# Kernel optimization log

Hardware: AMD Instinct MI355X
Metric: run time of the kernel (lower is better)

## Reference

```python
import jax, jax.numpy as jnp
import numpy as np

N = 1024          # number of rois (single image)
C = 1024          # in_channels
G = 16            # num_groups
PE = 64           # position_embedding_channels
WAVE_LENGTH = 1000.0


def _position_embedding(bboxes, pe_channels, wave_length):
    # bboxes: [N, 4] xyxy. Pairwise geometric features vs all (nongt == all) boxes.
    x1, y1, x2, y2 = jnp.split(bboxes, 4, axis=1)          # each [N,1]
    cx = (x1 + x2) * 0.5
    cy = (y1 + y2) * 0.5
    w = x2 - x1 + 1.0
    h = y2 - y1 + 1.0
    dX = jnp.log(jnp.clip(jnp.abs((cx - cx.T) / w), 1e-3))  # [N,N]
    dY = jnp.log(jnp.clip(jnp.abs((cy - cy.T) / h), 1e-3))
    dW = jnp.log(w / w.T)
    dH = jnp.log(h / h.T)
    pm = jnp.stack([dX, dY, dW, dH], axis=-1)               # [N,N,4]
    feat_range = jnp.arange(pe_channels // 8, dtype=pm.dtype)
    dim_mat = jnp.power(jnp.asarray(wave_length, pm.dtype),
                        (8.0 / pe_channels) * feat_range)    # [pe//8]
    div = (100.0 * pm)[..., None] / dim_mat                  # [N,N,4,pe//8]
    emb = jnp.concatenate([jnp.sin(div), jnp.cos(div)], axis=3)  # [N,N,4,pe//4]
    return emb.reshape(emb.shape[0], emb.shape[1], -1)       # [N,N,pe]


def setup_inputs() -> dict:
    key = jax.random.key(0)
    ks = jax.random.split(key, 10)
    feats = jax.random.normal(ks[0], (N, C), dtype=jnp.float32)
    # realistic boxes: x1,y1 in [0,800), w,h in [1,200)
    x1 = jax.random.uniform(ks[1], (N, 1), minval=0.0, maxval=800.0)
    y1 = jax.random.uniform(ks[2], (N, 1), minval=0.0, maxval=800.0)
    bw = jax.random.uniform(ks[3], (N, 1), minval=1.0, maxval=200.0)
    bh = jax.random.uniform(ks[4], (N, 1), minval=1.0, maxval=200.0)
    rois = jnp.concatenate([jnp.zeros((N, 1)), x1, y1, x1 + bw, y1 + bh], axis=1).astype(jnp.float32)
    Wq = 0.01 * jax.random.normal(ks[5], (C, C), dtype=jnp.float32)
    bq = jnp.zeros((C,), jnp.float32)
    Wk = 0.01 * jax.random.normal(ks[6], (C, C), dtype=jnp.float32)
    bk = jnp.zeros((C,), jnp.float32)
    Wg = 0.01 * jax.random.normal(ks[7], (G, PE), dtype=jnp.float32)   # 1x1 conv PE->G
    bg = jnp.zeros((G,), jnp.float32)
    # grouped 1x1 conv: in=G*C, out=C, groups=G -> weight [C, C]
    limit = np.sqrt(6.0 / (C + C))
    Wv = jax.random.uniform(ks[8], (C, C), minval=-limit, maxval=limit, dtype=jnp.float32)
    bv = jnp.zeros((C,), jnp.float32)
    return {"feats": feats, "rois": rois, "Wq": Wq, "bq": bq, "Wk": Wk, "bk": bk,
            "Wg": Wg, "bg": bg, "Wv": Wv, "bv": bv}


def reference(feats, rois, Wq, bq, Wk, bk, Wg, bg, Wv, bv):
    n, c = feats.shape
    g = Wg.shape[0]
    gc = c // g
    # position embedding computed under no_grad in torch
    emb = jax.lax.stop_gradient(_position_embedding(rois[:, 1:5], Wg.shape[1], WAVE_LENGTH))  # [N,N,PE]
    # 1x1 conv w_g + relu -> geometric attention weight [N, G, M]
    aff_weight = jax.nn.relu(jnp.einsum('nmp,gp->ngm', emb, Wg) + bg[None, :, None])
    q = (feats @ Wq.T + bq).reshape(n, g, gc)   # [N,G,gc]
    k = (feats @ Wk.T + bk).reshape(n, g, gc)   # [M,G,gc] (nongt == all)
    scale = 1.0 / jnp.sqrt(jnp.asarray(gc, jnp.float32))
    aff = jnp.einsum('ngc,mgc->ngm', q, k) * scale            # [N,G,M]
    weighted = jnp.log(jnp.clip(aff_weight, 1e-6)) + aff
    sm = jax.nn.softmax(weighted, axis=2)                      # [N,G,M]
    out = jnp.einsum('ngm,mc->ngc', sm, feats)                 # [N,G,C]
    # grouped 1x1 conv w_v: group g maps its C-dim aggregate to gc channels
    Wv_g = Wv.reshape(g, gc, c)
    rel = jnp.einsum('ngc,gdc->ngd', out, Wv_g).reshape(n, c) + bv
    return rel
```

## Files before the change

### kernel.cpp

```cpp
#include <hip/hip_runtime.h>
#include <math.h>

#define N_ROIS 1024
#define C_DIM  1024

typedef __attribute__((ext_vector_type(8))) short short8;
typedef __attribute__((ext_vector_type(4))) float f32x4;

__device__ __forceinline__ unsigned short f2bf(float x) {
    union { float f; unsigned u; } v; v.f = x;
    unsigned r = v.u + 0x7fffu + ((v.u >> 16) & 1u);
    return (unsigned short)(r >> 16);
}
__device__ __forceinline__ float bf2f(unsigned short u) {
    return __uint_as_float((unsigned)u << 16);
}
__device__ __forceinline__ unsigned cvtpk(float lo, float hi) {
    unsigned r;
    asm("v_cvt_pk_bf16_f32 %0, %1, %2" : "=v"(r) : "v"(lo), "v"(hi));
    return r;
}

__global__ __launch_bounds__(256) void cvt_kernel(
    const float* __restrict__ s0, const float* __restrict__ s1,
    const float* __restrict__ s2, const float* __restrict__ s3,
    unsigned short* __restrict__ d0, unsigned short* __restrict__ d1,
    unsigned short* __restrict__ d2, unsigned short* __restrict__ d3)
{
    const float* s; unsigned short* d;
    switch (blockIdx.y) {
        case 0:  s = s0; d = d0; break;
        case 1:  s = s1; d = d1; break;
        case 2:  s = s2; d = d2; break;
        default: s = s3; d = d3; break;
    }
    const int i = (blockIdx.x * 256 + threadIdx.x) * 8;
    float4 a = *(const float4*)&s[i];
    float4 b = *(const float4*)&s[i + 4];
    uint4 o;
    o.x = cvtpk(a.x, a.y); o.y = cvtpk(a.z, a.w);
    o.z = cvtpk(b.x, b.y); o.w = cvtpk(b.z, b.w);
    *(uint4*)&d[i] = o;
}

struct Triples {
    const unsigned short* A[3];
    const unsigned short* B[3];
    unsigned short*       C[3];
    const float*          bias[3];
};

__global__ __launch_bounds__(256) void prep_kernel(
    Triples tr, const float* __restrict__ rois, const float* __restrict__ Wg,
    const float* __restrict__ bg, unsigned short* __restrict__ logw)
{
    __shared__ __align__(16) char smem[52224];
    const int bx = blockIdx.x;
    const int t  = threadIdx.x;

    if (bx < 192) {
        constexpr int LDT = 40;
        unsigned short* As = (unsigned short*)smem;
        unsigned short* Bs = As + 128 * LDT;
        const int z   = bx >> 6;
        const int rem = bx & 63;
        const int m0 = (rem >> 3) * 128, n0 = (rem & 7) * 128;
        const unsigned short* A = tr.A[z];
        const unsigned short* B = tr.B[z];
        f32x4 acc[4][4];
        const f32x4 z4 = {0.f, 0.f, 0.f, 0.f};
#pragma unroll
        for (int i = 0; i < 4; ++i)
#pragma unroll
            for (int j = 0; j < 4; ++j) acc[i][j] = z4;

        const int row = t >> 2;
        const int kc  = (t & 3) * 8;
        const unsigned short* gA0 = A + (size_t)(m0 + row) * 1024 + kc;
        const unsigned short* gA1 = gA0 + (size_t)64 * 1024;
        unsigned short* sA0 = &As[row * LDT + kc];
        unsigned short* sA1 = sA0 + 64 * LDT;
        const unsigned short* gB0 = B + (size_t)(n0 + row) * 1024 + kc;
        const unsigned short* gB1 = gB0 + (size_t)64 * 1024;
        unsigned short* sB0 = &Bs[row * LDT + kc];
        unsigned short* sB1 = sB0 + 64 * LDT;
        int4 ra0 = *(const int4*)gA0;
        int4 ra1 = *(const int4*)gA1;
        int4 rb0 = *(const int4*)gB0;
        int4 rb1 = *(const int4*)gB1;
        const int lane = t & 63, wid = t >> 6;
        const int wm = (wid & 1) * 64, wn = (wid >> 1) * 64;
        const unsigned short* pa = &As[(wm + (lane & 15)) * LDT + (lane >> 4) * 8];
        const unsigned short* pb = &Bs[(wn + (lane & 15)) * LDT + (lane >> 4) * 8];
        for (int k0 = 0; k0 < 1024; k0 += 32) {
            *(int4*)sA0 = ra0; *(int4*)sA1 = ra1;
            *(int4*)sB0 = rb0; *(int4*)sB1 = rb1;
            __syncthreads();
            if (k0 + 32 < 1024) {
                ra0 = *(const int4*)(gA0 + k0 + 32);
                ra1 = *(const int4*)(gA1 + k0 + 32);
                rb0 = *(const int4*)(gB0 + k0 + 32);
                rb1 = *(const int4*)(gB1 + k0 + 32);
            }
            short8 af[4], bfr[4];
#pragma unroll
            for (int mi = 0; mi < 4; ++mi) af[mi]  = *(const short8*)(pa + mi * 16 * LDT);
#pragma unroll
            for (int ni = 0; ni < 4; ++ni) bfr[ni] = *(const short8*)(pb + ni * 16 * LDT);
#pragma unroll
            for (int mi = 0; mi < 4; ++mi)
#pragma unroll
                for (int ni = 0; ni < 4; ++ni)
                    acc[mi][ni] = __builtin_amdgcn_mfma_f32_16x16x32_bf16(
                        af[mi], bfr[ni], acc[mi][ni], 0, 0, 0);
            __syncthreads();
        }
        const float* bias = tr.bias[z];
        unsigned short* C = tr.C[z];
        const float sc = (z == 0) ? 0.125f : 1.0f;
        const int r0 = (lane >> 4) * 4, cc = lane & 15;
#pragma unroll
        for (int mi = 0; mi < 4; ++mi)
#pragma unroll
            for (int ni = 0; ni < 4; ++ni) {
                const int col = n0 + wn + ni * 16 + cc;
                const float bb = bias ? bias[col] : 0.f;
                const int rowi = m0 + wm + mi * 16 + r0;
                const unsigned p01 = cvtpk((acc[mi][ni][0] + bb) * sc,
                                           (acc[mi][ni][1] + bb) * sc);
                const unsigned p23 = cvtpk((acc[mi][ni][2] + bb) * sc,
                                           (acc[mi][ni][3] + bb) * sc);
                C[(size_t)rowi * 1024 + col]       = (unsigned short)(p01 & 0xffff);
                C[(size_t)(rowi + 1) * 1024 + col] = (unsigned short)(p01 >> 16);
                C[(size_t)(rowi + 2) * 1024 + col] = (unsigned short)(p23 & 0xffff);
                C[(size_t)(rowi + 3) * 1024 + col] = (unsigned short)(p23 >> 16);
            }
    } else {
        unsigned short* wg_s = (unsigned short*)smem;
        float* bg_s = (float*)(smem + 2304);
        float (*mbox)[4] = (float(*)[4])(smem + 2368);
        const int w = t >> 6, lane = t & 63;
        unsigned short* ptile = (unsigned short*)(smem + 18752) + w * 4160;
        if (t < 128) {
            const int gi = t >> 3, c = (t & 7) * 8;
            unsigned short* d = &wg_s[gi * 72 + c];
#pragma unroll
            for (int u = 0; u < 8; ++u) d[u] = f2bf(Wg[gi * 64 + c + u]);
        }
        if (t < 16) bg_s[t] = bg[t];
#pragma unroll
        for (int i = 0; i < 4; ++i) {
            const int m = t + i * 256;
            const float x1 = rois[m * 5 + 1], y1 = rois[m * 5 + 2];
            const float x2 = rois[m * 5 + 3], y2 = rois[m * 5 + 4];
            mbox[m][0] = (x1 + x2) * 0.5f;
            mbox[m][1] = (y1 + y2) * 0.5f;
            mbox[m][2] = __logf(x2 - x1 + 1.f);
            mbox[m][3] = __logf(y2 - y1 + 1.f);
        }
        const int n = bx - 192;
        const float x1 = rois[n * 5 + 1], y1 = rois[n * 5 + 2];
        const float x2 = rois[n * 5 + 3], y2 = rois[n * 5 + 4];
        const float cxn = (x1 + x2) * 0.5f, cyn = (y1 + y2) * 0.5f;
        const float wn = x2 - x1 + 1.f, hn = y2 - y1 + 1.f;
        const float iwn = 1.f / wn, ihn = 1.f / hn;
        const float lwn = __logf(wn), lhn = __logf(hn);
        __syncthreads();

        const int g  = lane & 15;
        const int qw = lane >> 4;
        const float coff = (qw & 1) ? 1.5707963268f : 0.f;
        const int f0 = qw >> 1;
        const short8 bf0 = *(const short8*)&wg_s[g * 72 + qw * 8];
        const short8 bf1 = *(const short8*)&wg_s[g * 72 + qw * 8 + 32];
        const float bgv = bg_s[g];
        const float invd[8] = {1.f, 0.42169650342f, 0.1778279410f, 0.07498942093f,
                               0.0316227766f, 0.01333521432f, 0.005623413252f, 0.002371373706f};

        for (int cl = 0; cl < 16; ++cl) {
            const int c  = w * 16 + cl;
            const int ma = c * 16 + g;
            float4 mb = *(const float4*)&mbox[ma][0];
            float p0 = (f0 == 0)
                     ? __logf(fmaxf(fabsf((cxn - mb.x) * iwn), 1e-3f))
                     : __logf(fmaxf(fabsf((cyn - mb.y) * ihn), 1e-3f));
            float p1 = (f0 == 0) ? (lwn - mb.z) : (lhn - mb.w);
            p0 *= 100.f; p1 *= 100.f;
            float s0v[8], s1v[8];
#pragma unroll
            for (int rr = 0; rr < 8; ++rr) {
                s0v[rr] = __sinf(p0 * invd[rr] + coff);
                s1v[rr] = __sinf(p1 * invd[rr] + coff);
            }
            union { uint4 u; short8 s; } a0, a1;
            a0.u.x = cvtpk(s0v[0], s0v[1]); a0.u.y = cvtpk(s0v[2], s0v[3]);
            a0.u.z = cvtpk(s0v[4], s0v[5]); a0.u.w = cvtpk(s0v[6], s0v[7]);
            a1.u.x = cvtpk(s1v[0], s1v[1]); a1.u.y = cvtpk(s1v[2], s1v[3]);
            a1.u.z = cvtpk(s1v[4], s1v[5]); a1.u.w = cvtpk(s1v[6], s1v[7]);
            f32x4 acc = {0.f, 0.f, 0.f, 0.f};
            acc = __builtin_amdgcn_mfma_f32_16x16x32_bf16(a0.s, bf0, acc, 0, 0, 0);
            acc = __builtin_amdgcn_mfma_f32_16x16x32_bf16(a1.s, bf1, acc, 0, 0, 0);
            const float l0 = __logf(fmaxf(acc[0] + bgv, 1e-6f));
            const float l1 = __logf(fmaxf(acc[1] + bgv, 1e-6f));
            const float l2 = __logf(fmaxf(acc[2] + bgv, 1e-6f));
            const float l3 = __logf(fmaxf(acc[3] + bgv, 1e-6f));
            uint2 pk;
            pk.x = cvtpk(l0, l1);
            pk.y = cvtpk(l2, l3);
            *(uint2*)&ptile[g * 260 + cl * 16 + qw * 4] = pk;
        }
        unsigned short* outp = logw + (size_t)n * 16384 + w * 256;
#pragma unroll
        for (int gg = 0; gg < 16; ++gg) {
            const uint2 pv = *(const uint2*)&ptile[gg * 260 + lane * 4];
            *(uint2*)&outp[gg * 1024 + lane * 4] = pv;
        }
    }
}

#define QOFF 0
#define KOFF 8192
#define FOFF 24576
#define LOFF 40960
#define POFF 57344
#define PPAD 72

__global__ __launch_bounds__(256) void attn_kernel(
    const unsigned short* __restrict__ qb, const unsigned short* __restrict__ kb,
    const unsigned short* __restrict__ logw, const unsigned short* __restrict__ FWt,
    const float* __restrict__ bv, float* __restrict__ out)
{
    __shared__ __align__(16) char smem[66560];

    const int t = threadIdx.x;
    const int bid = blockIdx.x;
    const int g  = (bid & 7) * 2 + ((bid >> 3) >> 4);
    const int n0 = ((bid >> 3) & 15) * 64;

    const int lane = t & 63, W = t >> 6;
    const int qw = lane >> 4, lx = lane & 15;
    const int lx7 = lx & 7;
    const int r8 = lane >> 3, u = lane & 7;

#define GLD(srcp, ldsoff) __builtin_amdgcn_global_load_lds( \
        (const __attribute__((address_space(1))) void*)(srcp), \
        (__attribute__((address_space(3))) void*)(smem + (ldsoff)), 16, 0, 0)

#pragma unroll
    for (int j = 0; j < 2; ++j) {
        const int c = W * 2 + j;
        const int r = c * 8 + r8;
        GLD(qb + (size_t)(n0 + r) * 1024 + g * 64 + ((u ^ (r & 7)) * 8),
            QOFF + c * 1024);
        GLD(kb + (size_t)r * 1024 + g * 64 + ((u ^ (r & 7)) * 8),
            KOFF + c * 1024);
        GLD(FWt + (size_t)(g * 64 + r) * 1024 + ((u ^ (r & 7)) * 8),
            FOFF + c * 1024);
        GLD(logw + (size_t)(n0 + r) * 16384 + g * 1024 + (((2 * u) ^ (r & 6)) * 4),
            LOFF + c * 1024);
    }
    __syncthreads();

    const unsigned short* qS = (const unsigned short*)(smem + QOFF);
    const int qrow = W * 16 + lx;
    const short8 bq0 = *(const short8*)(qS + qrow * 64 + ((qw ^ lx7) * 8));
    const short8 bq1 = *(const short8*)(qS + qrow * 64 + (((qw + 4) ^ lx7) * 8));
    unsigned short* Pw = (unsigned short*)(smem + POFF) + W * 16 * PPAD;

    f32x4 acc[4];
    const f32x4 z4 = {0.f, 0.f, 0.f, 0.f};
#pragma unroll
    for (int nb = 0; nb < 4; ++nb) acc[nb] = z4;
    float mrow = -1e30f, srow = 0.f;

    for (int i = 0; i < 16; ++i) {
        const int cur = i & 1;
        if (i < 15) {
            const int mc = (i + 1) * 64;
            const int nxt = cur ^ 1;
#pragma unroll
            for (int j = 0; j < 2; ++j) {
                const int c = W * 2 + j;
                const int r = c * 8 + r8;
                GLD(kb + (size_t)(mc + r) * 1024 + g * 64 + ((u ^ (r & 7)) * 8),
                    KOFF + nxt * 8192 + c * 1024);
                GLD(FWt + (size_t)(g * 64 + r) * 1024 + mc + ((u ^ (r & 7)) * 8),
                    FOFF + nxt * 8192 + c * 1024);
                GLD(logw + (size_t)(n0 + r) * 16384 + g * 1024 + mc
                        + (((2 * u) ^ (r & 6)) * 4),
                    LOFF + nxt * 8192 + c * 1024);
            }
        }

        const unsigned short* Kc = (const unsigned short*)(smem + KOFF + cur * 8192);
        const unsigned short* Fc = (const unsigned short*)(smem + FOFF + cur * 8192);
        const unsigned short* Lc = (const unsigned short*)(smem + LOFF + cur * 8192);

        f32x4 s[4];
#pragma unroll
        for (int tt = 0; tt < 4; ++tt) {
            const unsigned short* kr = Kc + (tt * 16 + lx) * 64;
            short8 a0 = *(const short8*)(kr + ((qw ^ lx7) * 8));
            short8 a1 = *(const short8*)(kr + (((qw + 4) ^ lx7) * 8));
            f32x4 z = z4;
            z = __builtin_amdgcn_mfma_f32_16x16x32_bf16(a0, bq0, z, 0, 0, 0);
            s[tt] = __builtin_amdgcn_mfma_f32_16x16x32_bf16(a1, bq1, z, 0, 0, 0);
        }

        const unsigned short* Lr = Lc + (W * 16 + lx) * 64;
        float v[4][4];
        float cmx = -1e30f;
#pragma unroll
        for (int tt = 0; tt < 4; ++tt) {
            const int off = ((tt * 32 + qw * 8) ^ ((lx & 6) << 3)) >> 1;
            const uint2 lw = *(const uint2*)(Lr + off);
            v[tt][0] = s[tt][0] + bf2f((unsigned short)(lw.x & 0xffff));
            v[tt][1] = s[tt][1] + bf2f((unsigned short)(lw.x >> 16));
            v[tt][2] = s[tt][2] + bf2f((unsigned short)(lw.y & 0xffff));
            v[tt][3] = s[tt][3] + bf2f((unsigned short)(lw.y >> 16));
            cmx = fmaxf(cmx, fmaxf(fmaxf(v[tt][0], v[tt][1]), fmaxf(v[tt][2], v[tt][3])));
        }
        cmx = fmaxf(cmx, __shfl_xor(cmx, 16));
        cmx = fmaxf(cmx, __shfl_xor(cmx, 32));

        const float nm = fmaxf(mrow, cmx);
        const float f  = __expf(mrow - nm);
        mrow = nm;
        srow *= f;
#pragma unroll
        for (int nb = 0; nb < 4; ++nb) {
            acc[nb][0] *= f; acc[nb][1] *= f;
            acc[nb][2] *= f; acc[nb][3] *= f;
        }

#pragma unroll
        for (int tt = 0; tt < 4; ++tt) {
            const float p0 = __expf(v[tt][0] - nm);
            const float p1 = __expf(v[tt][1] - nm);
            const float p2 = __expf(v[tt][2] - nm);
            const float p3 = __expf(v[tt][3] - nm);
            srow += (p0 + p1) + (p2 + p3);
            uint2 pk;
            pk.x = cvtpk(p0, p1);
            pk.y = cvtpk(p2, p3);
            *(uint2*)&Pw[lx * PPAD + tt * 16 + qw * 4] = pk;
        }

#pragma unroll
        for (int ks = 0; ks < 2; ++ks) {
            const short8 ap = *(const short8*)&Pw[lx * PPAD + ks * 32 + qw * 8];
#pragma unroll
            for (int nb = 0; nb < 4; ++nb) {
                const unsigned short* fr = Fc + (nb * 16 + lx) * 64;
                short8 fb = *(const short8*)(fr + (((ks * 4 + qw) ^ lx7) * 8));
                acc[nb] = __builtin_amdgcn_mfma_f32_16x16x32_bf16(fb, ap, acc[nb], 0, 0, 0);
            }
        }

        __syncthreads();
    }

    srow += __shfl_xor(srow, 16);
    srow += __shfl_xor(srow, 32);
    const float inv = 1.f / srow;
    float* Ow = (float*)smem + W * 16 * 68;
#pragma unroll
    for (int nb = 0; nb < 4; ++nb)
#pragma unroll
        for (int r = 0; r < 4; ++r)
            Ow[lx * 68 + nb * 16 + qw * 4 + r] = acc[nb][r] * inv;
    {
        const int row = lane >> 2, d0 = (lane & 3) * 16;
        const float* Orow = (float*)smem + W * 16 * 68 + row * 68;
        float* op = out + (size_t)(n0 + W * 16 + row) * 1024 + g * 64 + d0;
#pragma unroll
        for (int j = 0; j < 4; ++j) {
            float4 o = *(const float4*)(Orow + d0 + j * 4);
            const float4 b4 = *(const float4*)&bv[g * 64 + d0 + j * 4];
            o.x += b4.x; o.y += b4.y; o.z += b4.z; o.w += b4.w;
            *(float4*)(op + j * 4) = o;
        }
    }
#undef GLD
}

extern "C" void kernel_launch(void* const* d_in, const int* in_sizes, int n_in,
                              void* d_out, int out_size, void* d_ws, size_t ws_size,
                              hipStream_t stream)
{
    const float* feats = (const float*)d_in[0];
    const float* rois  = (const float*)d_in[1];
    const float* Wq    = (const float*)d_in[2];
    const float* bq    = (const float*)d_in[3];
    const float* Wk    = (const float*)d_in[4];
    const float* bk    = (const float*)d_in[5];
    const float* Wg    = (const float*)d_in[6];
    const float* bg    = (const float*)d_in[7];
    const float* Wv    = (const float*)d_in[8];
    const float* bv    = (const float*)d_in[9];
    float* out = (float*)d_out;

    char* wsb = (char*)d_ws;
    unsigned short* logwb  = (unsigned short*)(wsb + (0ull  << 20));
    unsigned short* featsb = (unsigned short*)(wsb + (64ull << 20));
    unsigned short* qb     = (unsigned short*)(wsb + (66ull << 20));
    unsigned short* kb     = (unsigned short*)(wsb + (68ull << 20));
    unsigned short* FWtb   = (unsigned short*)(wsb + (70ull << 20));
    unsigned short* Wqb    = (unsigned short*)(wsb + (80ull << 20));
    unsigned short* Wkb    = (unsigned short*)(wsb + (82ull << 20));
    unsigned short* Wvb    = (unsigned short*)(wsb + (84ull << 20));

    cvt_kernel<<<dim3(512, 4), 256, 0, stream>>>(feats, Wq, Wk, Wv,
                                                 featsb, Wqb, Wkb, Wvb);

    Triples tr;
    tr.A[0] = featsb; tr.B[0] = Wqb;    tr.C[0] = qb;   tr.bias[0] = bq;
    tr.A[1] = featsb; tr.B[1] = Wkb;    tr.C[1] = kb;   tr.bias[1] = bk;
    tr.A[2] = Wvb;    tr.B[2] = featsb; tr.C[2] = FWtb; tr.bias[2] = nullptr;
    prep_kernel<<<1216, 256, 0, stream>>>(tr, rois, Wg, bg, logwb);

    attn_kernel<<<256, 256, 0, stream>>>(qb, kb, logwb, FWtb, bv, out);
}
```

Baseline: 64.93 us.

## Fuse weight bf16 conversion into GEMM loads and split position embedding kernel

Drops the separate conversion kernel. Weights are now converted from fp32 to bf16 inside the GEMM load path, and the feats conversion moves into a new position-embedding kernel. The old combined prep kernel is split in two: a 1024-block pos_kernel, with each block handling four rois against a 256-column slice, and a separate 8x8x3 GEMM kernel that depends on featsb. This removes a pass that wrote bf16 weights out and read them back, but the GEMM now reads fp32 weights (double the bytes), and the GEMMs no longer run concurrently with the embedding work in the same launch.

```diff
diff --git a/kernel.cpp b/kernel.cpp
--- a/kernel.cpp
+++ b/kernel.cpp
@@ -20,202 +20,222 @@
     asm("v_cvt_pk_bf16_f32 %0, %1, %2" : "=v"(r) : "v"(lo), "v"(hi));
     return r;
 }
-
-__global__ __launch_bounds__(256) void cvt_kernel(
-    const float* __restrict__ s0, const float* __restrict__ s1,
-    const float* __restrict__ s2, const float* __restrict__ s3,
-    unsigned short* __restrict__ d0, unsigned short* __restrict__ d1,
-    unsigned short* __restrict__ d2, unsigned short* __restrict__ d3)
+__device__ __forceinline__ int4 ldcvt(const float* p) {
+    float4 f0 = *(const float4*)p;
+    float4 f1 = *(const float4*)(p + 4);
+    int4 r;
+    r.x = (int)cvtpk(f0.x, f0.y); r.y = (int)cvtpk(f0.z, f0.w);
+    r.z = (int)cvtpk(f1.x, f1.y); r.w = (int)cvtpk(f1.z, f1.w);
+    return r;
+}
+
+__global__ __launch_bounds__(256) void pos_kernel(
+    const float* __restrict__ rois, const float* __restrict__ Wg,
+    const float* __restrict__ bg, const float* __restrict__ feats,
+    unsigned short* __restrict__ featsb, unsigned short* __restrict__ logw)
 {
-    const float* s; unsigned short* d;
-    switch (blockIdx.y) {
-        case 0:  s = s0; d = d0; break;
-        case 1:  s = s1; d = d1; break;
-        case 2:  s = s2; d = d2; break;
-        default: s = s3; d = d3; break;
-    }
-    const int i = (blockIdx.x * 256 + threadIdx.x) * 8;
-    float4 a = *(const float4*)&s[i];
-    float4 b = *(const float4*)&s[i + 4];
-    uint4 o;
-    o.x = cvtpk(a.x, a.y); o.y = cvtpk(a.z, a.w);
-    o.z = cvtpk(b.x, b.y); o.w = cvtpk(b.z, b.w);
-    *(uint4*)&d[i] = o;
-}
-
-struct Triples {
-    const unsigned short* A[3];
-    const unsigned short* B[3];
-    unsigned short*       C[3];
-    const float*          bias[3];
+    __shared__ unsigned short wg_s[16 * 72];
+    __shared__ float bg_s[16];
+    __shared__ float mbox[256][4];
+    __shared__ unsigned short ptile[4][2240];
+
+    const int t  = threadIdx.x;
+    const int pb = blockIdx.x;
+    const int ngrp = pb >> 2;
+    const int mc   = (pb & 3) * 256;
+    const int lane = t & 63, w = t >> 6;
+    const int g = lane & 15, qw = lane >> 4;
+
+    {
+        const int i = pb * 1024 + t * 4;
+        float4 a = *(const float4*)&feats[i];
+        uint2 o;
+        o.x = cvtpk(a.x, a.y); o.y = cvtpk(a.z, a.w);
+        *(uint2*)&featsb[i] = o;
+    }
+
+    if (t < 128) {
+        const int gi = t >> 3, c = (t & 7) * 8;
+        unsigned short* d = &wg_s[gi * 72 + c];
+#pragma unroll
+        for (int u2 = 0; u2 < 8; ++u2) d[u2] = f2bf(Wg[gi * 64 + c + u2]);
+    }
+    if (t < 16) bg_s[t] = bg[t];
+    {
+        const int m = mc + t;
+        const float x1 = rois[m * 5 + 1], y1 = rois[m * 5 + 2];
+        const float x2 = rois[m * 5 + 3], y2 = rois[m * 5 + 4];
+        mbox[t][0] = (x1 + x2) * 0.5f;
+        mbox[t][1] = (y1 + y2) * 0.5f;
+        mbox[t][2] = __logf(x2 - x1 + 1.f);
+        mbox[t][3] = __logf(y2 - y1 + 1.f);
+    }
+    const int n = ngrp * 4 + w;
+    const float x1 = rois[n * 5 + 1], y1 = rois[n * 5 + 2];
+    const float x2 = rois[n * 5 + 3], y2 = rois[n * 5 + 4];
+    const float cxn = (x1 + x2) * 0.5f, cyn = (y1 + y2) * 0.5f;
+    const float wn = x2 - x1 + 1.f, hn = y2 - y1 + 1.f;
+    const float iwn = 1.f / wn, ihn = 1.f / hn;
+    const float lwn = __logf(wn), lhn = __logf(hn);
+    __syncthreads();
+
+    const float coff = (qw & 1) ? 1.5707963268f : 0.f;
+    const int f0 = qw >> 1;
+    const short8 bf0 = *(const short8*)&wg_s[g * 72 + qw * 8];
+    const short8 bf1 = *(const short8*)&wg_s[g * 72 + qw * 8 + 32];
+    const float bgv = bg_s[g];
+    const float invd[8] = {1.f, 0.42169650342f, 0.1778279410f, 0.07498942093f,
+                           0.0316227766f, 0.01333521432f, 0.005623413252f, 0.002371373706f};
+    unsigned short* pt = ptile[w];
+
+    for (int cl = 0; cl < 16; ++cl) {
+        float4 mb = *(const float4*)&mbox[cl * 16 + g][0];
+        float p0 = (f0 == 0)
+                 ? __logf(fmaxf(fabsf((cxn - mb.x) * iwn), 1e-3f))
+                 : __logf(fmaxf(fabsf((cyn - mb.y) * ihn), 1e-3f));
+        float p1 = (f0 == 0) ? (lwn - mb.z) : (lhn - mb.w);
+        p0 *= 100.f; p1 *= 100.f;
+        float s0v[8], s1v[8];
+#pragma unroll
+        for (int rr = 0; rr < 8; ++rr) {
+            s0v[rr] = __sinf(p0 * invd[rr] + coff);
+            s1v[rr] = __sinf(p1 * invd[rr] + coff);
+        }
+        union { uint4 u; short8 s; } a0, a1;
+        a0.u.x = cvtpk(s0v[0], s0v[1]); a0.u.y = cvtpk(s0v[2], s0v[3]);
+        a0.u.z = cvtpk(s0v[4], s0v[5]); a0.u.w = cvtpk(s0v[6], s0v[7]);
+        a1.u.x = cvtpk(s1v[0], s1v[1]); a1.u.y = cvtpk(s1v[2], s1v[3]);
+        a1.u.z = cvtpk(s1v[4], s1v[5]); a1.u.w = cvtpk(s1v[6], s1v[7]);
+        f32x4 acc = {0.f, 0.f, 0.f, 0.f};
+        acc = __builtin_amdgcn_mfma_f32_16x16x32_bf16(a0.s, bf0, acc, 0, 0, 0);
+        acc = __builtin_amdgcn_mfma_f32_16x16x32_bf16(a1.s, bf1, acc, 0, 0, 0);
+        const float l0 = __logf(fmaxf(acc[0] + bgv, 1e-6f));
+        const float l1 = __logf(fmaxf(acc[1] + bgv, 1e-6f));
+        const float l2 = __logf(fmaxf(acc[2] + bgv, 1e-6f));
+        const float l3 = __logf(fmaxf(acc[3] + bgv, 1e-6f));
+        uint2 pk;
+        pk.x = cvtpk(l0, l1);
+        pk.y = cvtpk(l2, l3);
+        *(uint2*)&pt[g * 140 + (cl & 7) * 16 + qw * 4] = pk;
+
+        if ((cl & 7) == 7) {
+            const int fl = cl >> 3;
+            const int gg = lane >> 2, c4 = lane & 3;
+            unsigned short* op = logw + (size_t)n * 16384 + gg * 1024 + mc + fl * 128;
+            const unsigned short* rp = &pt[gg * 140];
+#pragma unroll
+            for (int j = 0; j < 8; ++j) {
+                const int mo = (c4 + j * 4) * 4;
+                *(uint2*)&op[mo] = *(const uint2*)&rp[mo];
+            }
+        }
+    }
+}
+
+struct GemmArgs {
+    const unsigned short* featsb;
+    const float* Wq; const float* Wk; const float* Wv;
+    const float* bq; const float* bk;
+    unsigned short* qb; unsigned short* kb; unsigned short* FWtb;
 };
 
-__global__ __launch_bounds__(256) void prep_kernel(
-    Triples tr, const float* __restrict__ rois, const float* __restrict__ Wg,
-    const float* __restrict__ bg, unsigned short* __restrict__ logw)
+__global__ __launch_bounds__(256) void gemm3_kernel(GemmArgs ga)
 {
-    __shared__ __align__(16) char smem[52224];
-    const int bx = blockIdx.x;
+    constexpr int LDT = 40;
+    __shared__ unsigned short As[128 * LDT];
+    __shared__ unsigned short Bs[128 * LDT];
+    const int z  = blockIdx.z;
+    const int m0 = blockIdx.y * 128, n0 = blockIdx.x * 128;
     const int t  = threadIdx.x;
-
-    if (bx < 192) {
-        constexpr int LDT = 40;
-        unsigned short* As = (unsigned short*)smem;
-        unsigned short* Bs = As + 128 * LDT;
-        const int z   = bx >> 6;
-        const int rem = bx & 63;
-        const int m0 = (rem >> 3) * 128, n0 = (rem & 7) * 128;
-        const unsigned short* A = tr.A[z];
-        const unsigned short* B = tr.B[z];
-        f32x4 acc[4][4];
-        const f32x4 z4 = {0.f, 0.f, 0.f, 0.f};
-#pragma unroll
-        for (int i = 0; i < 4; ++i)
-#pragma unroll
-            for (int j = 0; j < 4; ++j) acc[i][j] = z4;
-
-        const int row = t >> 2;
-        const int kc  = (t & 3) * 8;
-        const unsigned short* gA0 = A + (size_t)(m0 + row) * 1024 + kc;
-        const unsigned short* gA1 = gA0 + (size_t)64 * 1024;
-        unsigned short* sA0 = &As[row * LDT + kc];
-        unsigned short* sA1 = sA0 + 64 * LDT;
-        const unsigned short* gB0 = B + (size_t)(n0 + row) * 1024 + kc;
-        const unsigned short* gB1 = gB0 + (size_t)64 * 1024;
-        unsigned short* sB0 = &Bs[row * LDT + kc];
-        unsigned short* sB1 = sB0 + 64 * LDT;
-        int4 ra0 = *(const int4*)gA0;
-        int4 ra1 = *(const int4*)gA1;
-        int4 rb0 = *(const int4*)gB0;
-        int4 rb1 = *(const int4*)gB1;
-        const int lane = t & 63, wid = t >> 6;
-        const int wm = (wid & 1) * 64, wn = (wid >> 1) * 64;
-        const unsigned short* pa = &As[(wm + (lane & 15)) * LDT + (lane >> 4) * 8];
-        const unsigned short* pb = &Bs[(wn + (lane & 15)) * LDT + (lane >> 4) * 8];
-        for (int k0 = 0; k0 < 1024; k0 += 32) {
-            *(int4*)sA0 = ra0; *(int4*)sA1 = ra1;
-            *(int4*)sB0 = rb0; *(int4*)sB1 = rb1;
-            __syncthreads();
-            if (k0 + 32 < 1024) {
-                ra0 = *(const int4*)(gA0 + k0 + 32);
-                ra1 = *(const int4*)(gA1 + k0 + 32);
-                rb0 = *(const int4*)(gB0 + k0 + 32);
-                rb1 = *(const int4*)(gB1 + k0 + 32);
+    const int row = t >> 2, kc = (t & 3) * 8;
+
+    f32x4 acc[4][4];
+    const f32x4 z4 = {0.f, 0.f, 0.f, 0.f};
+#pragma unroll
+    for (int i = 0; i < 4; ++i)
+#pragma unroll
+        for (int j = 0; j < 4; ++j) acc[i][j] = z4;
+
+    const unsigned short* bA0 = ga.featsb + (size_t)(m0 + row) * 1024 + kc;
+    const unsigned short* bA1 = bA0 + (size_t)64 * 1024;
+    const unsigned short* bB0 = ga.featsb + (size_t)(n0 + row) * 1024 + kc;
+    const unsigned short* bB1 = bB0 + (size_t)64 * 1024;
+    const float* fW = (z == 0) ? ga.Wq : (z == 1) ? ga.Wk : ga.Wv;
+    const float* fA0 = fW + (size_t)(m0 + row) * 1024 + kc;
+    const float* fA1 = fA0 + (size_t)64 * 1024;
+    const float* fB0 = fW + (size_t)(n0 + row) * 1024 + kc;
+    const float* fB1 = fB0 + (size_t)64 * 1024;
+
+    unsigned short* sA0 = &As[row * LDT + kc];
+    unsigned short* sA1 = sA0 + 64 * LDT;
+    unsigned short* sB0 = &Bs[row * LDT + kc];
+    unsigned short* sB1 = sB0 + 64 * LDT;
+
+    int4 ra0, ra1, rb0, rb1;
+    if (z == 2) {
+        ra0 = ldcvt(fA0);            ra1 = ldcvt(fA1);
+        rb0 = *(const int4*)bB0;     rb1 = *(const int4*)bB1;
+    } else {
+        ra0 = *(const int4*)bA0;     ra1 = *(const int4*)bA1;
+        rb0 = ldcvt(fB0);            rb1 = ldcvt(fB1);
+    }
+
+    const int lane = t & 63, wid = t >> 6;
+    const int wm = (wid & 1) * 64, wn = (wid >> 1) * 64;
+    const unsigned short* pa = &As[(wm + (lane & 15)) * LDT + (lane >> 4) * 8];
+    const unsigned short* pb = &Bs[(wn + (lane & 15)) * LDT + (lane >> 4) * 8];
+
+    for (int k0 = 0; k0 < 1024; k0 += 32) {
+        *(int4*)sA0 = ra0; *(int4*)sA1 = ra1;
+        *(int4*)sB0 = rb0; *(int4*)sB1 = rb1;
+        __syncthreads();
+        if (k0 + 32 < 1024) {
+            if (z == 2) {
+                ra0 = ldcvt(fA0 + k0 + 32);
+                ra1 = ldcvt(fA1 + k0 + 32);
+                rb0 = *(const int4*)(bB0 + k0 + 32);
+                rb1 = *(const int4*)(bB1 + k0 + 32);
+            } else {
+                ra0 = *(const int4*)(bA0 + k0 + 32);
+                ra1 = *(const int4*)(bA1 + k0 + 32);
+                rb0 = ldcvt(fB0 + k0 + 32);
+                rb1 = ldcvt(fB1 + k0 + 32);
             }
-            short8 af[4], bfr[4];
-#pragma unroll
-            for (int mi = 0; mi < 4; ++mi) af[mi]  = *(const short8*)(pa + mi * 16 * LDT);
-#pragma unroll
-            for (int ni = 0; ni < 4; ++ni) bfr[ni] = *(const short8*)(pb + ni * 16 * LDT);
-#pragma unroll
-            for (int mi = 0; mi < 4; ++mi)
-#pragma unroll
-                for (int ni = 0; ni < 4; ++ni)
-                    acc[mi][ni] = __builtin_amdgcn_mfma_f32_16x16x32_bf16(
-                        af[mi], bfr[ni], acc[mi][ni], 0, 0, 0);
-            __syncthreads();
-        }
-        const float* bias = tr.bias[z];
-        unsigned short* C = tr.C[z];
-        const float sc = (z == 0) ? 0.125f : 1.0f;
-        const int r0 = (lane >> 4) * 4, cc = lane & 15;
+        }
+        short8 af[4], bfr[4];
+#pragma unroll
+        for (int mi = 0; mi < 4; ++mi) af[mi]  = *(const short8*)(pa + mi * 16 * LDT);
+#pragma unroll
+        for (int ni = 0; ni < 4; ++ni) bfr[ni] = *(const short8*)(pb + ni * 16 * LDT);
 #pragma unroll
         for (int mi = 0; mi < 4; ++mi)
 #pragma unroll
-            for (int ni = 0; ni < 4; ++ni) {
-                const int col = n0 + wn + ni * 16 + cc;
-                const float bb = bias ? bias[col] : 0.f;
-                const int rowi = m0 + wm + mi * 16 + r0;
-                const unsigned p01 = cvtpk((acc[mi][ni][0] + bb) * sc,
-                                           (acc[mi][ni][1] + bb) * sc);
-                const unsigned p23 = cvtpk((acc[mi][ni][2] + bb) * sc,
-                                           (acc[mi][ni][3] + bb) * sc);
-                C[(size_t)rowi * 1024 + col]       = (unsigned short)(p01 & 0xffff);
-                C[(size_t)(rowi + 1) * 1024 + col] = (unsigned short)(p01 >> 16);
-                C[(size_t)(rowi + 2) * 1024 + col] = (unsigned short)(p23 & 0xffff);
-                C[(size_t)(rowi + 3) * 1024 + col] = (unsigned short)(p23 >> 16);
-            }
-    } else {
-        unsigned short* wg_s = (unsigned short*)smem;
-        float* bg_s = (float*)(smem + 2304);
-        float (*mbox)[4] = (float(*)[4])(smem + 2368);
-        const int w = t >> 6, lane = t & 63;
-        unsigned short* ptile = (unsigned short*)(smem + 18752) + w * 4160;
-        if (t < 128) {
-            const int gi = t >> 3, c = (t & 7) * 8;
-            unsigned short* d = &wg_s[gi * 72 + c];
-#pragma unroll
-            for (int u = 0; u < 8; ++u) d[u] = f2bf(Wg[gi * 64 + c + u]);
-        }
-        if (t < 16) bg_s[t] = bg[t];
-#pragma unroll
-        for (int i = 0; i < 4; ++i) {
-            const int m = t + i * 256;
-            const float x1 = rois[m * 5 + 1], y1 = rois[m * 5 + 2];
-            const float x2 = rois[m * 5 + 3], y2 = rois[m * 5 + 4];
-            mbox[m][0] = (x1 + x2) * 0.5f;
-            mbox[m][1] = (y1 + y2) * 0.5f;
-            mbox[m][2] = __logf(x2 - x1 + 1.f);
-            mbox[m][3] = __logf(y2 - y1 + 1.f);
-        }
-        const int n = bx - 192;
-        const float x1 = rois[n * 5 + 1], y1 = rois[n * 5 + 2];
-        const float x2 = rois[n * 5 + 3], y2 = rois[n * 5 + 4];
-        const float cxn = (x1 + x2) * 0.5f, cyn = (y1 + y2) * 0.5f;
-        const float wn = x2 - x1 + 1.f, hn = y2 - y1 + 1.f;
-        const float iwn = 1.f / wn, ihn = 1.f / hn;
-        const float lwn = __logf(wn), lhn = __logf(hn);
+            for (int ni = 0; ni < 4; ++ni)
+                acc[mi][ni] = __builtin_amdgcn_mfma_f32_16x16x32_bf16(
+                    af[mi], bfr[ni], acc[mi][ni], 0, 0, 0);
         __syncthreads();
-
-        const int g  = lane & 15;
-        const int qw = lane >> 4;
-        const float coff = (qw & 1) ? 1.5707963268f : 0.f;
-        const int f0 = qw >> 1;
-        const short8 bf0 = *(const short8*)&wg_s[g * 72 + qw * 8];
-        const short8 bf1 = *(const short8*)&wg_s[g * 72 + qw * 8 + 32];
-        const float bgv = bg_s[g];
-        const float invd[8] = {1.f, 0.42169650342f, 0.1778279410f, 0.07498942093f,
-                               0.0316227766f, 0.01333521432f, 0.005623413252f, 0.002371373706f};
-
-        for (int cl = 0; cl < 16; ++cl) {
-            const int c  = w * 16 + cl;
-            const int ma = c * 16 + g;
-            float4 mb = *(const float4*)&mbox[ma][0];
-            float p0 = (f0 == 0)
-                     ? __logf(fmaxf(fabsf((cxn - mb.x) * iwn), 1e-3f))
-                     : __logf(fmaxf(fabsf((cyn - mb.y) * ihn), 1e-3f));
-            float p1 = (f0 == 0) ? (lwn - mb.z) : (lhn - mb.w);
-            p0 *= 100.f; p1 *= 100.f;
-            float s0v[8], s1v[8];
-#pragma unroll
-            for (int rr = 0; rr < 8; ++rr) {
-                s0v[rr] = __sinf(p0 * invd[rr] + coff);
-                s1v[rr] = __sinf(p1 * invd[rr] + coff);
-            }
-            union { uint4 u; short8 s; } a0, a1;
-            a0.u.x = cvtpk(s0v[0], s0v[1]); a0.u.y = cvtpk(s0v[2], s0v[3]);
-            a0.u.z = cvtpk(s0v[4], s0v[5]); a0.u.w = cvtpk(s0v[6], s0v[7]);
-            a1.u.x = cvtpk(s1v[0], s1v[1]); a1.u.y = cvtpk(s1v[2], s1v[3]);
-            a1.u.z = cvtpk(s1v[4], s1v[5]); a1.u.w = cvtpk(s1v[6], s1v[7]);
-            f32x4 acc = {0.f, 0.f, 0.f, 0.f};
-            acc = __builtin_amdgcn_mfma_f32_16x16x32_bf16(a0.s, bf0, acc, 0, 0, 0);
-            acc = __builtin_amdgcn_mfma_f32_16x16x32_bf16(a1.s, bf1, acc, 0, 0, 0);
-            const float l0 = __logf(fmaxf(acc[0] + bgv, 1e-6f));
-            const float l1 = __logf(fmaxf(acc[1] + bgv, 1e-6f));
-            const float l2 = __logf(fmaxf(acc[2] + bgv, 1e-6f));
-            const float l3 = __logf(fmaxf(acc[3] + bgv, 1e-6f));
-            uint2 pk;
-            pk.x = cvtpk(l0, l1);
-            pk.y = cvtpk(l2, l3);
-            *(uint2*)&ptile[g * 260 + cl * 16 + qw * 4] = pk;
-        }
-        unsigned short* outp = logw + (size_t)n * 16384 + w * 256;
-#pragma unroll
-        for (int gg = 0; gg < 16; ++gg) {
-            const uint2 pv = *(const uint2*)&ptile[gg * 260 + lane * 4];
-            *(uint2*)&outp[gg * 1024 + lane * 4] = pv;
-        }
-    }
+    }
+
+    const float* bias = (z == 0) ? ga.bq : (z == 1) ? ga.bk : nullptr;
+    unsigned short* C = (z == 0) ? ga.qb : (z == 1) ? ga.kb : ga.FWtb;
+    const float sc = (z == 0) ? 0.125f : 1.0f;
+    const int r0 = (lane >> 4) * 4, cc = lane & 15;
+#pragma unroll
+    for (int mi = 0; mi < 4; ++mi)
+#pragma unroll
+        for (int ni = 0; ni < 4; ++ni) {
+            const int col = n0 + wn + ni * 16 + cc;
+            const float bb = bias ? bias[col] : 0.f;
+            const int rowi = m0 + wm + mi * 16 + r0;
+            const unsigned p01 = cvtpk((acc[mi][ni][0] + bb) * sc,
+                                       (acc[mi][ni][1] + bb) * sc);
+            const unsigned p23 = cvtpk((acc[mi][ni][2] + bb) * sc,
+                                       (acc[mi][ni][3] + bb) * sc);
+            C[(size_t)rowi * 1024 + col]       = (unsigned short)(p01 & 0xffff);
+            C[(size_t)(rowi + 1) * 1024 + col] = (unsigned short)(p01 >> 16);
+            C[(size_t)(rowi + 2) * 1024 + col] = (unsigned short)(p23 & 0xffff);
+            C[(size_t)(rowi + 3) * 1024 + col] = (unsigned short)(p23 >> 16);
+        }
 }
 
 #define QOFF 0
@@ -406,18 +426,15 @@
     unsigned short* qb     = (unsigned short*)(wsb + (66ull << 20));
     unsigned short* kb     = (unsigned short*)(wsb + (68ull << 20));
     unsigned short* FWtb   = (unsigned short*)(wsb + (70ull << 20));
-    unsigned short* Wqb    = (unsigned short*)(wsb + (80ull << 20));
-    unsigned short* Wkb    = (unsigned short*)(wsb + (82ull << 20));
-    unsigned short* Wvb    = (unsigned short*)(wsb + (84ull << 20));
-
-    cvt_kernel<<<dim3(512, 4), 256, 0, stream>>>(feats, Wq, Wk, Wv,
-                                                 featsb, Wqb, Wkb, Wvb);
-
-    Triples tr;
-    tr.A[0] = featsb; tr.B[0] = Wqb;    tr.C[0] = qb;   tr.bias[0] = bq;
-    tr.A[1] = featsb; tr.B[1] = Wkb;    tr.C[1] = kb;   tr.bias[1] = bk;
-    tr.A[2] = Wvb;    tr.B[2] = featsb; tr.C[2] = FWtb; tr.bias[2] = nullptr;
-    prep_kernel<<<1216, 256, 0, stream>>>(tr, rois, Wg, bg, logwb);
+
+    pos_kernel<<<1024, 256, 0, stream>>>(rois, Wg, bg, feats, featsb, logwb);
+
+    GemmArgs ga;
+    ga.featsb = featsb;
+    ga.Wq = Wq; ga.Wk = Wk; ga.Wv = Wv;
+    ga.bq = bq; ga.bk = bk;
+    ga.qb = qb; ga.kb = kb; ga.FWtb = FWtb;
+    gemm3_kernel<<<dim3(8, 8, 3), 256, 0, stream>>>(ga);
 
     attn_kernel<<<256, 256, 0, stream>>>(qb, kb, logwb, FWtb, bv, out);
 }
```

New measurement: 85.02 us. 1.31x slower.

## Shrink prep-kernel LDS and interleave GEMM tiles with position-embedding blocks

Applied to the files above, without the earlier changes.

Each embedding block now handles four rois (one per wave) against a 256-box slice instead of one roi against all 1024 boxes. This cuts the shared-memory footprint from about 52KB to about 24KB so more blocks fit per CU. GEMM tile blocks are interleaved with embedding blocks (3 of every 19) to spread the heavier GEMM work across the grid. Output staging is flushed every 8 chunks with a smaller tile, trading more frequent small global writes for lower LDS use.

```diff
diff --git a/kernel.cpp b/kernel.cpp
--- a/kernel.cpp
+++ b/kernel.cpp
@@ -54,17 +54,19 @@
     Triples tr, const float* __restrict__ rois, const float* __restrict__ Wg,
     const float* __restrict__ bg, unsigned short* __restrict__ logw)
 {
-    __shared__ __align__(16) char smem[52224];
+    __shared__ __align__(16) char smem[24448];
     const int bx = blockIdx.x;
     const int t  = threadIdx.x;
-
-    if (bx < 192) {
+    const int grp = bx / 19, rem = bx % 19;
+
+    if (rem < 3) {
         constexpr int LDT = 40;
         unsigned short* As = (unsigned short*)smem;
         unsigned short* Bs = As + 128 * LDT;
-        const int z   = bx >> 6;
-        const int rem = bx & 63;
-        const int m0 = (rem >> 3) * 128, n0 = (rem & 7) * 128;
+        const int gid = grp * 3 + rem;
+        const int z   = gid >> 6;
+        const int r2  = gid & 63;
+        const int m0 = (r2 >> 3) * 128, n0 = (r2 & 7) * 128;
         const unsigned short* A = tr.A[z];
         const unsigned short* B = tr.B[z];
         f32x4 acc[4][4];
@@ -139,26 +141,31 @@
         unsigned short* wg_s = (unsigned short*)smem;
         float* bg_s = (float*)(smem + 2304);
         float (*mbox)[4] = (float(*)[4])(smem + 2368);
-        const int w = t >> 6, lane = t & 63;
-        unsigned short* ptile = (unsigned short*)(smem + 18752) + w * 4160;
+        unsigned short* ptile0 = (unsigned short*)(smem + 6464);
+        const int pb = grp * 16 + (rem - 3);
+        const int ngrp = pb >> 2;
+        const int mc   = (pb & 3) * 256;
+        const int lane = t & 63, w = t >> 6;
+        const int g = lane & 15, qw = lane >> 4;
+        unsigned short* pt = ptile0 + w * 2240;
+
         if (t < 128) {
             const int gi = t >> 3, c = (t & 7) * 8;
             unsigned short* d = &wg_s[gi * 72 + c];
 #pragma unroll
-            for (int u = 0; u < 8; ++u) d[u] = f2bf(Wg[gi * 64 + c + u]);
+            for (int u2 = 0; u2 < 8; ++u2) d[u2] = f2bf(Wg[gi * 64 + c + u2]);
         }
         if (t < 16) bg_s[t] = bg[t];
-#pragma unroll
-        for (int i = 0; i < 4; ++i) {
-            const int m = t + i * 256;
+        {
+            const int m = mc + t;
             const float x1 = rois[m * 5 + 1], y1 = rois[m * 5 + 2];
             const float x2 = rois[m * 5 + 3], y2 = rois[m * 5 + 4];
-            mbox[m][0] = (x1 + x2) * 0.5f;
-            mbox[m][1] = (y1 + y2) * 0.5f;
-            mbox[m][2] = __logf(x2 - x1 + 1.f);
-            mbox[m][3] = __logf(y2 - y1 + 1.f);
-        }
-        const int n = bx - 192;
+            mbox[t][0] = (x1 + x2) * 0.5f;
+            mbox[t][1] = (y1 + y2) * 0.5f;
+            mbox[t][2] = __logf(x2 - x1 + 1.f);
+            mbox[t][3] = __logf(y2 - y1 + 1.f);
+        }
+        const int n = ngrp * 4 + w;
         const float x1 = rois[n * 5 + 1], y1 = rois[n * 5 + 2];
         const float x2 = rois[n * 5 + 3], y2 = rois[n * 5 + 4];
         const float cxn = (x1 + x2) * 0.5f, cyn = (y1 + y2) * 0.5f;
@@ -167,8 +174,6 @@
         const float lwn = __logf(wn), lhn = __logf(hn);
         __syncthreads();
 
-        const int g  = lane & 15;
-        const int qw = lane >> 4;
         const float coff = (qw & 1) ? 1.5707963268f : 0.f;
         const int f0 = qw >> 1;
         const short8 bf0 = *(const short8*)&wg_s[g * 72 + qw * 8];
@@ -178,9 +183,7 @@
                                0.0316227766f, 0.01333521432f, 0.005623413252f, 0.002371373706f};
 
         for (int cl = 0; cl < 16; ++cl) {
-            const int c  = w * 16 + cl;
-            const int ma = c * 16 + g;
-            float4 mb = *(const float4*)&mbox[ma][0];
+            float4 mb = *(const float4*)&mbox[cl * 16 + g][0];
             float p0 = (f0 == 0)
                      ? __logf(fmaxf(fabsf((cxn - mb.x) * iwn), 1e-3f))
                      : __logf(fmaxf(fabsf((cyn - mb.y) * ihn), 1e-3f));
@@ -207,13 +210,19 @@
             uint2 pk;
             pk.x = cvtpk(l0, l1);
             pk.y = cvtpk(l2, l3);
-            *(uint2*)&ptile[g * 260 + cl * 16 + qw * 4] = pk;
-        }
-        unsigned short* outp = logw + (size_t)n * 16384 + w * 256;
-#pragma unroll
-        for (int gg = 0; gg < 16; ++gg) {
-            const uint2 pv = *(const uint2*)&ptile[gg * 260 + lane * 4];
-            *(uint2*)&outp[gg * 1024 + lane * 4] = pv;
+            *(uint2*)&pt[g * 140 + (cl & 7) * 16 + qw * 4] = pk;
+
+            if ((cl & 7) == 7) {
+                const int fl = cl >> 3;
+                const int gg = lane >> 2, c4 = lane & 3;
+                unsigned short* op = logw + (size_t)n * 16384 + gg * 1024 + mc + fl * 128;
+                const unsigned short* rp = &pt[gg * 140];
+#pragma unroll
+                for (int j = 0; j < 8; ++j) {
+                    const int mo = (c4 + j * 4) * 4;
+                    *(uint2*)&op[mo] = *(const uint2*)&rp[mo];
+                }
+            }
         }
     }
 }
```

Measured after the change: 71.92 us. 1.11x slower.
